# Performance work log

Hardware: AMD Instinct MI355X
Metric: run time of the kernel (lower is better)

The kernel has to match this reference:

```python
import jax, jax.numpy as jnp
import numpy as np

B, N = 1, 512
C_S, C_Z, C_HID, H, P_Q, P_V = 384, 128, 16, 12, 4, 8
W_C = (2.0 / (9.0 * P_Q)) ** 0.5
W_L = (1.0 / 3.0) ** 0.5
F_IN = H * C_Z + H * C_HID + H * P_V * 3 + H * P_V  # 2112


def setup_inputs() -> dict:
    key = jax.random.key(0)
    ks = jax.random.split(key, 14)
    s_i = jax.random.normal(ks[0], (B, N, C_S), jnp.float32)
    z_ij = jax.random.normal(ks[1], (B, N, N, C_Z), jnp.float32)
    # proper rotation matrices via QR so invert_apply is a true rigid inverse
    rot, _ = jnp.linalg.qr(jax.random.normal(ks[2], (B, N, 3, 3), jnp.float32))
    trans = jax.random.normal(ks[3], (B, N, 3), jnp.float32)
    sc = lambda fan: 1.0 / np.sqrt(fan)
    Wq = jax.random.normal(ks[4], (C_S, H, C_HID), jnp.float32) * sc(C_S)
    Wk = jax.random.normal(ks[5], (C_S, H, C_HID), jnp.float32) * sc(C_S)
    Wv = jax.random.normal(ks[6], (C_S, H, C_HID), jnp.float32) * sc(C_S)
    Wqp = jax.random.normal(ks[7], (C_S, H, P_Q, 3), jnp.float32) * sc(C_S)
    Wkp = jax.random.normal(ks[8], (C_S, H, P_Q, 3), jnp.float32) * sc(C_S)
    Wvp = jax.random.normal(ks[9], (C_S, H, P_V, 3), jnp.float32) * sc(C_S)
    Wb = jax.random.normal(ks[10], (C_Z, H), jnp.float32) * sc(C_Z)
    gamma = jax.random.normal(ks[11], (H,), jnp.float32)
    Wf = jax.random.normal(ks[12], (F_IN, C_S), jnp.float32) * sc(F_IN)
    bf = jnp.zeros((C_S,), jnp.float32)
    return {"s_i": s_i, "z_ij": z_ij, "rot": rot, "trans": trans,
            "Wq": Wq, "Wk": Wk, "Wv": Wv, "Wqp": Wqp, "Wkp": Wkp, "Wvp": Wvp,
            "Wb": Wb, "gamma": gamma, "Wf": Wf, "bf": bf}


def _apply(rot, trans, p):
    # rigid transform per residue: R_i @ p + t_i ; p: (B,N,H,P,3)
    return jnp.einsum('bimn,bihpn->bihpm', rot, p) + trans[:, :, None, None, :]


def reference(s_i, z_ij, rot, trans, Wq, Wk, Wv, Wqp, Wkp, Wvp, Wb, gamma, Wf, bf):
    q = jnp.einsum('bic,chd->bihd', s_i, Wq)            # (B,N,H,C_HID)
    k = jnp.einsum('bic,chd->bihd', s_i, Wk)
    v = jnp.einsum('bic,chd->bihd', s_i, Wv)
    qp = jnp.einsum('bic,chpx->bihpx', s_i, Wqp)        # (B,N,H,Pq,3)
    kp = jnp.einsum('bic,chpx->bihpx', s_i, Wkp)
    vp = jnp.einsum('bic,chpx->bihpx', s_i, Wvp)        # (B,N,H,Pv,3)
    b_ij = jnp.einsum('bijc,ch->bijh', z_ij, Wb)        # pair bias (B,N,N,H)

    qp_g = _apply(rot, trans, qp)
    kp_g = _apply(rot, trans, kp)
    # squared global point distances, summed over points: (B,N,N,H)
    d2 = jnp.sum((qp_g[:, :, None] - kp_g[:, None]) ** 2, axis=(-1, -2))

    qk = jnp.einsum('bihd,bjhd->bijh', q, k) * (1.0 / np.sqrt(C_HID))
    logits = W_L * (qk + b_ij - (W_C * 0.5) * gamma * d2)
    a = jax.nn.softmax(logits, axis=2)                  # softmax over j

    o_pair = jnp.einsum('bijh,bijc->bihc', a, z_ij)     # (B,N,H,C_Z)
    o_sc = jnp.einsum('bijh,bjhd->bihd', a, v)          # (B,N,H,C_HID)
    vp_g = _apply(rot, trans, vp)
    o_pt_g = jnp.einsum('bijh,bjhpx->bihpx', a, vp_g)   # (B,N,H,Pv,3)
    # invert_apply at residue i: R_i^T @ (x - t_i)
    o_pt = jnp.einsum('bimn,bihpm->bihpn', rot, o_pt_g - trans[:, :, None, None, :])
    o_norm = jnp.sqrt(jnp.sum(o_pt ** 2, axis=-1) + 1e-12)  # (B,N,H,Pv)

    feat = jnp.concatenate([o_pair.reshape(B, N, -1), o_sc.reshape(B, N, -1),
                            o_pt.reshape(B, N, -1), o_norm.reshape(B, N, -1)], axis=-1)
    return feat @ Wf + bf
```

## Files before the change

kernel.cpp:

```cpp
#include <hip/hip_runtime.h>
#include <hip/hip_bf16.h>
#include <math.h>

#define Nn    512
#define CS    384
#define CZ    128
#define CH    16
#define Hh    12
#define PQ    4
#define PV    8
#define NCOL  1152
#define FIN   2112

#define W_C   0.23570226039551584f
#define W_L   0.5773502691896258f

typedef unsigned short ushort_t;
typedef unsigned int uint_t;
typedef __attribute__((ext_vector_type(8))) short bf16x8;
typedef __attribute__((ext_vector_type(4))) float f32x4;

#define OFF_P      0u
#define OFF_MQ     589824u
#define OFF_MK     595968u
#define OFF_VT     602112u
#define OFF_VPT    651264u
#define OFF_S16    1830912u
#define OFF_WCT    1929216u
#define OFF_WFT    2150400u
#define OFF_F16    2555904u
#define OFF_PP     3145728u
#define OFF_VFRAG  5328896u
#define OFF_EXT    5451776u
#define OFF_EKB    21755904u
#define OFF_EQB    21854208u
#define OFF_WBF    21952512u

__device__ inline ushort_t f2bf(float f) {
  __hip_bfloat16 h = __float2bfloat16(f);
  return *reinterpret_cast<ushort_t*>(&h);
}
__device__ inline float bf2f(ushort_t u) {
  unsigned int x = ((unsigned int)u) << 16;
  return __uint_as_float(x);
}

__global__ __launch_bounds__(384) void k_conv(
    const float* __restrict__ s, const float* __restrict__ Wq,
    const float* __restrict__ Wk, const float* __restrict__ Wv,
    const float* __restrict__ Wqp, const float* __restrict__ Wkp,
    const float* __restrict__ Wvp, const float* __restrict__ Wf,
    const float* __restrict__ Wb,
    ushort_t* __restrict__ s16, ushort_t* __restrict__ WcatT,
    ushort_t* __restrict__ WfT, ushort_t* __restrict__ wbf) {
  int b = blockIdx.x;
  if (b < 512) {
    int idx = b * 384 + threadIdx.x;
    s16[idx] = f2bf(s[idx]);
  } else if (b < 1664) {
    int col = b - 512, k = threadIdx.x;
    float v;
    if      (col < 192)  v = Wq [k * 192 + col];
    else if (col < 384)  v = Wk [k * 192 + col - 192];
    else if (col < 576)  v = Wv [k * 192 + col - 384];
    else if (col < 720)  v = Wqp[k * 144 + col - 576];
    else if (col < 864)  v = Wkp[k * 144 + col - 720];
    else                 v = Wvp[k * 288 + col - 864];
    WcatT[(size_t)col * CS + k] = f2bf(v);
  } else if (b < 2048) {
    int o = b - 1664;
    for (int f = threadIdx.x; f < FIN; f += 384)
      WfT[(size_t)o * FIN + f] = f2bf(Wf[(size_t)f * CS + o]);
  } else {
    int t = threadIdx.x;
    if (t < 256) {
      int kk = t >> 6, l = t & 63;
      int h = l & 15, lk = l >> 4;
#pragma unroll
      for (int e = 0; e < 8; ++e) {
        int c = kk * 32 + lk * 8 + e;
        wbf[t * 8 + e] = (h < Hh) ? f2bf(Wb[c * Hh + h]) : (ushort_t)0;
      }
    }
  }
}

__global__ __launch_bounds__(64) void k_projm(
    const ushort_t* __restrict__ s16, const ushort_t* __restrict__ WcatT,
    float* __restrict__ P) {
  int colt = blockIdx.x;
  int i0 = blockIdx.y * 16;
  int l = threadIdx.x;
  int cl = l & 15, lk = l >> 4;
  f32x4 accA = {0.f, 0.f, 0.f, 0.f}, accB = {0.f, 0.f, 0.f, 0.f};
  const ushort_t* arow = s16 + (size_t)(i0 + cl) * CS;
  const ushort_t* brow = WcatT + (size_t)(colt * 16 + cl) * CS;
#pragma unroll
  for (int kk = 0; kk < 12; kk += 2) {
    bf16x8 a0 = *(const bf16x8*)(arow + kk * 32 + lk * 8);
    bf16x8 b0 = *(const bf16x8*)(brow + kk * 32 + lk * 8);
    accA = __builtin_amdgcn_mfma_f32_16x16x32_bf16(a0, b0, accA, 0, 0, 0);
    bf16x8 a1 = *(const bf16x8*)(arow + (kk + 1) * 32 + lk * 8);
    bf16x8 b1 = *(const bf16x8*)(brow + (kk + 1) * 32 + lk * 8);
    accB = __builtin_amdgcn_mfma_f32_16x16x32_bf16(a1, b1, accB, 0, 0, 0);
  }
#pragma unroll
  for (int r = 0; r < 4; ++r)
    P[(size_t)(i0 + lk * 4 + r) * NCOL + colt * 16 + cl] = accA[r] + accB[r];
}

__global__ __launch_bounds__(64) void k_prep(
    const float* __restrict__ P, const float* __restrict__ rot,
    const float* __restrict__ trans, const float* __restrict__ gamma,
    ushort_t* __restrict__ eqb, ushort_t* __restrict__ ekb,
    float* __restrict__ mq, float* __restrict__ mk,
    ushort_t* __restrict__ vT, ushort_t* __restrict__ vpT) {
  int gid = blockIdx.x * 64 + threadIdx.x;
  int i = gid / Hh, h = gid % Hh;
  const float* Pi = P + (size_t)i * NCOL;
  float R[9], T[3];
#pragma unroll
  for (int m = 0; m < 9; ++m) R[m] = rot[i * 9 + m];
#pragma unroll
  for (int m = 0; m < 3; ++m) T[m] = trans[i * 3 + m];
  float cg = W_C * gamma[h];

  ushort_t* eq = eqb + (size_t)gid * 32;
  ushort_t* ek = ekb + (size_t)gid * 32;
#pragma unroll
  for (int d = 0; d < CH; ++d) eq[d] = f2bf(Pi[h * CH + d] * 0.25f);
#pragma unroll
  for (int d = 0; d < CH; ++d) ek[d] = f2bf(Pi[192 + h * CH + d]);
  float sq = 0.f, sk = 0.f;
#pragma unroll
  for (int p = 0; p < PQ; ++p) {
    float x = Pi[576 + h * 12 + p * 3 + 0];
    float y = Pi[576 + h * 12 + p * 3 + 1];
    float zc = Pi[576 + h * 12 + p * 3 + 2];
    float gx = R[0] * x + R[1] * y + R[2] * zc + T[0];
    float gy = R[3] * x + R[4] * y + R[5] * zc + T[1];
    float gz = R[6] * x + R[7] * y + R[8] * zc + T[2];
    eq[16 + p * 3 + 0] = f2bf(cg * gx);
    eq[16 + p * 3 + 1] = f2bf(cg * gy);
    eq[16 + p * 3 + 2] = f2bf(cg * gz);
    sq += gx * gx + gy * gy + gz * gz;
  }
#pragma unroll
  for (int p = 0; p < PQ; ++p) {
    float x = Pi[720 + h * 12 + p * 3 + 0];
    float y = Pi[720 + h * 12 + p * 3 + 1];
    float zc = Pi[720 + h * 12 + p * 3 + 2];
    float gx = R[0] * x + R[1] * y + R[2] * zc + T[0];
    float gy = R[3] * x + R[4] * y + R[5] * zc + T[1];
    float gz = R[6] * x + R[7] * y + R[8] * zc + T[2];
    ek[16 + p * 3 + 0] = f2bf(gx);
    ek[16 + p * 3 + 1] = f2bf(gy);
    ek[16 + p * 3 + 2] = f2bf(gz);
    sk += gx * gx + gy * gy + gz * gz;
  }
#pragma unroll
  for (int d = 28; d < 32; ++d) { eq[d] = 0; ek[d] = 0; }
  mq[gid] = -0.5f * cg * sq;
  mk[gid] = -0.5f * cg * sk;

#pragma unroll
  for (int d = 0; d < CH; ++d)
    vT[(size_t)(h * CH + d) * Nn + i] = f2bf(Pi[384 + h * CH + d]);
#pragma unroll
  for (int p = 0; p < PV; ++p) {
    float x = Pi[864 + h * 24 + p * 3 + 0];
    float y = Pi[864 + h * 24 + p * 3 + 1];
    float zc = Pi[864 + h * 24 + p * 3 + 2];
    vpT[(size_t)(h * 24 + p * 3 + 0) * Nn + i] = f2bf(R[0] * x + R[1] * y + R[2] * zc + T[0]);
    vpT[(size_t)(h * 24 + p * 3 + 1) * Nn + i] = f2bf(R[3] * x + R[4] * y + R[5] * zc + T[1]);
    vpT[(size_t)(h * 24 + p * 3 + 2) * Nn + i] = f2bf(R[6] * x + R[7] * y + R[8] * zc + T[2]);
  }
}

__global__ __launch_bounds__(768) void k_aux(
    const ushort_t* __restrict__ eqb, const ushort_t* __restrict__ ekb,
    const float* __restrict__ mk, float* __restrict__ ext,
    const ushort_t* __restrict__ vT, const ushort_t* __restrict__ vpT,
    ushort_t* __restrict__ vfrag) {
  int b = blockIdx.x, tid = threadIdx.x;
  if (b < 1024) {
    int it = b >> 5, jt = b & 31;
    int l = tid & 63, h = tid >> 6;
    int cl = l & 15, lk = l >> 4;
    bf16x8 a = *(const bf16x8*)(eqb + ((size_t)(it * 16 + cl) * Hh + h) * 32 + lk * 8);
    bf16x8 bb = *(const bf16x8*)(ekb + ((size_t)(jt * 16 + cl) * Hh + h) * 32 + lk * 8);
    f32x4 dl = {0.f, 0.f, 0.f, 0.f};
    dl = __builtin_amdgcn_mfma_f32_16x16x32_bf16(a, bb, dl, 0, 0, 0);
    float mkv = mk[(jt * 16 + cl) * Hh + h];
    float* erow = ext + ((size_t)h * Nn + it * 16 + lk * 4) * Nn + jt * 16 + cl;
#pragma unroll
    for (int r = 0; r < 4; ++r) erow[(size_t)r * Nn] = dl[r] + mkv;
  } else {
    int flat = (b - 1024) * 768 + tid;
    if (flat < 30720) {
      int tt = flat >> 10;
      int r = flat & 1023;
      int jb = r >> 6, l = r & 63;
      int cl = l & 15, lk = l >> 4;
      const ushort_t* src = (tt < 12)
          ? vT  + (size_t)(tt * 16 + cl) * Nn
          : vpT + (size_t)((tt - 12) * 16 + cl) * Nn;
      bf16x8 v = *(const bf16x8*)(src + jb * 32 + lk * 8);
      *(bf16x8*)(vfrag + (((size_t)tt * 16 + jb) * 64 + l) * 8) = v;
    }
  }
}

__global__ __launch_bounds__(512, 4) void k_fused9(
    const float* __restrict__ z, const ushort_t* __restrict__ wbf,
    const float* __restrict__ ext, const ushort_t* __restrict__ vfrag,
    float* __restrict__ pp) {
  __shared__ float smemf[20240];
  char*     ztc  = (char*)smemf;
  char*     pB   = (char*)smemf + 65536;
  ushort_t* extb = (ushort_t*)((char*)smemf + 73728);
  float*    mb   = smemf + 19968;
  float*    lb   = smemf + 20096;
  float*    Mv   = smemf + 20224;

  int i = blockIdx.x, half = blockIdx.y, tid = threadIdx.x;
  int l = tid & 63, w = tid >> 6;
  int cl = l & 15, lk = l >> 4;
  int j0b = half * 256;
  float* po = pp + ((size_t)i * 2 + half) * 2048;
  int swz = (cl & 7) << 4;

  const float4* zg4 = (const float4*)(z + ((size_t)i * Nn + j0b) * CZ);
  float4 xv0 = zg4[w * 1024 + 0 * 64 + l],  xv1 = zg4[w * 1024 + 1 * 64 + l];
  float4 xv2 = zg4[w * 1024 + 2 * 64 + l],  xv3 = zg4[w * 1024 + 3 * 64 + l];
  float4 xv4 = zg4[w * 1024 + 4 * 64 + l],  xv5 = zg4[w * 1024 + 5 * 64 + l];
  float4 xv6 = zg4[w * 1024 + 6 * 64 + l],  xv7 = zg4[w * 1024 + 7 * 64 + l];
  float4 xv8 = zg4[w * 1024 + 8 * 64 + l],  xv9 = zg4[w * 1024 + 9 * 64 + l];
  float4 xv10 = zg4[w * 1024 + 10 * 64 + l], xv11 = zg4[w * 1024 + 11 * 64 + l];
  float4 xv12 = zg4[w * 1024 + 12 * 64 + l], xv13 = zg4[w * 1024 + 13 * 64 + l];
  float4 xv14 = zg4[w * 1024 + 14 * 64 + l], xv15 = zg4[w * 1024 + 15 * 64 + l];
  float ev[6];
#pragma unroll
  for (int q = 0; q < 6; ++q) {
    int flat = q * 64 + l;
    int eh = flat >> 5, ejl = flat & 31;
    ev[q] = ext[((size_t)eh * Nn + i) * Nn + j0b + w * 32 + ejl];
  }

#define STORE_ZT(it_, xv_) { \
    int idxl = (it_) * 64 + l; \
    int row = w * 32 + (idxl >> 5), c4 = idxl & 31; \
    uint2 pk; \
    pk.x = (uint_t)f2bf(xv_.x) | ((uint_t)f2bf(xv_.y) << 16); \
    pk.y = (uint_t)f2bf(xv_.z) | ((uint_t)f2bf(xv_.w) << 16); \
    *(uint2*)&ztc[row * 256 + ((c4 * 8) ^ ((row & 7) << 4))] = pk; }
  STORE_ZT(0, xv0)   STORE_ZT(1, xv1)   STORE_ZT(2, xv2)   STORE_ZT(3, xv3)
  STORE_ZT(4, xv4)   STORE_ZT(5, xv5)   STORE_ZT(6, xv6)   STORE_ZT(7, xv7)
  STORE_ZT(8, xv8)   STORE_ZT(9, xv9)   STORE_ZT(10, xv10) STORE_ZT(11, xv11)
  STORE_ZT(12, xv12) STORE_ZT(13, xv13) STORE_ZT(14, xv14) STORE_ZT(15, xv15)
#undef STORE_ZT
#pragma unroll
  for (int q = 0; q < 6; ++q) {
    int flat = q * 64 + l;
    extb[(w * 32 + (flat & 31)) * 12 + (flat >> 5)] = f2bf(ev[q]);
  }

  bf16x8 wbreg[4];
#pragma unroll
  for (int kk = 0; kk < 4; ++kk)
    wbreg[kk] = *(const bf16x8*)&wbf[(kk * 64 + l) * 8];

  float v[2][4];
#pragma unroll
  for (int cg = 0; cg < 2; ++cg) {
    int jloc = w * 32 + cg * 16 + cl;
    f32x4 dl = {0.f, 0.f, 0.f, 0.f};
#pragma unroll
    for (int kk = 0; kk < 4; ++kk) {
      bf16x8 a = *(const bf16x8*)&ztc[jloc * 256 + ((kk * 64 + lk * 16) ^ ((cl & 7) << 4))];
      dl = __builtin_amdgcn_mfma_f32_16x16x32_bf16(a, wbreg[kk], dl, 0, 0, 0);
    }
    if (cl < Hh) {
#pragma unroll
      for (int r = 0; r < 4; ++r)
        v[cg][r] = W_L * (dl[r] +
            bf2f(extb[(w * 32 + cg * 16 + lk * 4 + r) * 12 + cl]));
    } else {
#pragma unroll
      for (int r = 0; r < 4; ++r) v[cg][r] = -1e30f;
    }
  }

  float m_w = v[0][0];
#pragma unroll
  for (int cg = 0; cg < 2; ++cg)
#pragma unroll
    for (int r = 0; r < 4; ++r) m_w = fmaxf(m_w, v[cg][r]);
  m_w = fmaxf(m_w, __shfl_xor(m_w, 16));
  m_w = fmaxf(m_w, __shfl_xor(m_w, 32));

  float ps = 0.f;
#pragma unroll
  for (int cg = 0; cg < 2; ++cg) {
    int j = w * 32 + cg * 16 + lk * 4;
    ushort_t p0 = f2bf(__expf(v[cg][0] - m_w));
    ushort_t p1 = f2bf(__expf(v[cg][1] - m_w));
    ushort_t p2 = f2bf(__expf(v[cg][2] - m_w));
    ushort_t p3 = f2bf(__expf(v[cg][3] - m_w));
    ps += bf2f(p0) + bf2f(p1) + bf2f(p2) + bf2f(p3);
    uint2 d;
    d.x = (uint_t)p0 | ((uint_t)p1 << 16);
    d.y = (uint_t)p2 | ((uint_t)p3 << 16);
    *(uint2*)&pB[(cl * 512 + j * 2) ^ swz] = d;
  }
  ps += __shfl_xor(ps, 16);
  ps += __shfl_xor(ps, 32);
  if (lk == 0) { mb[w * 16 + cl] = m_w; lb[w * 16 + cl] = ps; }
  __syncthreads();

  if (tid < 16) {
    float M = mb[tid];
#pragma unroll
    for (int ww = 1; ww < 8; ++ww) M = fmaxf(M, mb[ww * 16 + tid]);
    float L = 0.f;
#pragma unroll
    for (int ww = 0; ww < 8; ++ww) L += lb[ww * 16 + tid] * __expf(mb[ww * 16 + tid] - M);
    Mv[tid] = M;
    po[2016 + tid] = M;
    po[2032 + tid] = L;
  }
  __syncthreads();

  float sf = __expf(m_w - Mv[cl]);
#pragma unroll
  for (int q = 0; q < 2; ++q) {
    int j = w * 32 + lk * 8 + q * 4;
    uint_t off = (uint_t)(cl * 512 + j * 2) ^ swz;
    uint2 d = *(uint2*)&pB[off];
    ushort_t q0 = f2bf(bf2f((ushort_t)(d.x & 0xffff)) * sf);
    ushort_t q1 = f2bf(bf2f((ushort_t)(d.x >> 16)) * sf);
    ushort_t q2 = f2bf(bf2f((ushort_t)(d.y & 0xffff)) * sf);
    ushort_t q3 = f2bf(bf2f((ushort_t)(d.y >> 16)) * sf);
    d.x = (uint_t)q0 | ((uint_t)q1 << 16);
    d.y = (uint_t)q2 | ((uint_t)q3 << 16);
    *(uint2*)&pB[off] = d;
  }
  __syncthreads();

  f32x4 acc[5];
#pragma unroll
  for (int n = 0; n < 5; ++n) acc[n] = (f32x4){0.f, 0.f, 0.f, 0.f};
  bf16x8 vA[4], vB[4];

#define LOADV(buf, kk_) { \
    _Pragma("unroll") \
    for (int n = 1; n < 5; ++n) { \
      int t = w + n * 8; \
      if (t < 38) buf[n - 1] = *(const bf16x8*)(vfrag + \
          (((size_t)(t - 8) * 16 + (half * 8 + (kk_))) * 64 + l) * 8); \
    } }
#define COMPUTE(buf, kk_) { \
    int koff = (kk_) * 32 + lk * 8; \
    bf16x8 af = *(const bf16x8*)&pB[(cl * 512 + koff * 2) ^ swz]; \
    bf16x8 b0; \
    _Pragma("unroll") \
    for (int e = 0; e < 8; ++e) \
      b0[e] = *(const short*)&ztc[(koff + e) * 256 + ((w * 32 + cl * 2) ^ (e << 4))]; \
    acc[0] = __builtin_amdgcn_mfma_f32_16x16x32_bf16(af, b0, acc[0], 0, 0, 0); \
    _Pragma("unroll") \
    for (int n = 1; n < 5; ++n) { \
      int t = w + n * 8; \
      if (t < 38) acc[n] = __builtin_amdgcn_mfma_f32_16x16x32_bf16(af, buf[n - 1], acc[n], 0, 0, 0); \
    } }

  LOADV(vA, 0)
#pragma unroll
  for (int kk = 0; kk < 8; kk += 2) {
    LOADV(vB, kk + 1)
    COMPUTE(vA, kk)
    if (kk < 6) LOADV(vA, kk + 2)
    COMPUTE(vB, kk + 1)
  }
#undef LOADV
#undef COMPUTE

#pragma unroll
  for (int n = 0; n < 5; ++n) {
    int t = w + n * 8;
    if (t < 38) {
      if (t < 8) {
        int c = t * 16 + cl;
#pragma unroll
        for (int r = 0; r < 4; ++r) {
          int h = lk * 4 + r;
          if (h < Hh) po[h * CZ + c] = acc[n][r];
        }
      } else if (t < 20) {
        int h = t - 8;
        if (lk == (h >> 2)) po[1536 + h * CH + cl] = acc[n][h & 3];
      } else {
        int cp = (t - 20) * 16 + cl;
        int h = cp / 24;
        if (lk == (h >> 2)) po[1728 + cp] = acc[n][h & 3];
      }
    }
  }
}

__global__ __launch_bounds__(256) void k_merge(
    const float* __restrict__ pp, const float* __restrict__ rot,
    const float* __restrict__ trans, ushort_t* __restrict__ feat16) {
  __shared__ float a0s[16], a1s[16];
  __shared__ float optg[288];
  int i = blockIdx.x, tid = threadIdx.x;
  const float* p0 = pp + ((size_t)i * 2 + 0) * 2048;
  const float* p1 = pp + ((size_t)i * 2 + 1) * 2048;
  ushort_t* Fi = feat16 + (size_t)i * FIN;

  if (tid < 16) {
    float m0 = p0[2016 + tid], m1 = p1[2016 + tid];
    float M = fmaxf(m0, m1);
    float s0 = __expf(m0 - M), s1 = __expf(m1 - M);
    float L = p0[2032 + tid] * s0 + p1[2032 + tid] * s1;
    float inv = (tid < Hh) ? 1.f / L : 0.f;
    a0s[tid] = s0 * inv;
    a1s[tid] = s1 * inv;
  }
  __syncthreads();

  for (int idx = tid; idx < 1728; idx += 256) {
    int h = (idx < 1536) ? (idx >> 7) : ((idx - 1536) >> 4);
    Fi[idx] = f2bf(p0[idx] * a0s[h] + p1[idx] * a1s[h]);
  }
  for (int idx = tid; idx < 288; idx += 256) {
    int h = idx / 24;
    optg[idx] = p0[1728 + idx] * a0s[h] + p1[1728 + idx] * a1s[h];
  }
  __syncthreads();

  if (tid < 96) {
    int h = tid >> 3, p = tid & 7;
    int cp = h * 24 + p * 3;
    float g0 = optg[cp + 0] - trans[i * 3 + 0];
    float g1 = optg[cp + 1] - trans[i * 3 + 1];
    float g2 = optg[cp + 2] - trans[i * 3 + 2];
    const float* R = rot + i * 9;
    float ss = 0.f;
#pragma unroll
    for (int nn2 = 0; nn2 < 3; ++nn2) {
      float o = R[nn2] * g0 + R[3 + nn2] * g1 + R[6 + nn2] * g2;
      Fi[1728 + cp + nn2] = f2bf(o);
      ss += o * o;
    }
    Fi[2016 + h * 8 + p] = f2bf(sqrtf(ss + 1e-12f));
  }
}

__global__ __launch_bounds__(256) void k_outm2(
    const ushort_t* __restrict__ feat16, const ushort_t* __restrict__ WfT,
    const float* __restrict__ bfv, float* __restrict__ out) {
  __shared__ f32x4 red[4][64];
  int ot = blockIdx.x;
  int ib = blockIdx.y;
  int tid = threadIdx.x;
  int l = tid & 63, w = tid >> 6;
  int cl = l & 15, lk = l >> 4;
  int i0 = ib * 32 + (w >> 1) * 16;
  int kw = w & 1;
  const ushort_t* arow = feat16 + (size_t)(i0 + cl) * FIN;
  const ushort_t* brow = WfT + (size_t)(ot * 16 + cl) * FIN;
  f32x4 accA = {0.f, 0.f, 0.f, 0.f}, accB = {0.f, 0.f, 0.f, 0.f};
  int k0 = kw * 33;
#pragma unroll 4
  for (int kk = k0; kk < k0 + 32; kk += 2) {
    bf16x8 a0 = *(const bf16x8*)(arow + kk * 32 + lk * 8);
    bf16x8 b0 = *(const bf16x8*)(brow + kk * 32 + lk * 8);
    accA = __builtin_amdgcn_mfma_f32_16x16x32_bf16(a0, b0, accA, 0, 0, 0);
    bf16x8 a1 = *(const bf16x8*)(arow + (kk + 1) * 32 + lk * 8);
    bf16x8 b1 = *(const bf16x8*)(brow + (kk + 1) * 32 + lk * 8);
    accB = __builtin_amdgcn_mfma_f32_16x16x32_bf16(a1, b1, accB, 0, 0, 0);
  }
  {
    int kk = k0 + 32;
    bf16x8 a = *(const bf16x8*)(arow + kk * 32 + lk * 8);
    bf16x8 b = *(const bf16x8*)(brow + kk * 32 + lk * 8);
    accA = __builtin_amdgcn_mfma_f32_16x16x32_bf16(a, b, accA, 0, 0, 0);
  }
#pragma unroll
  for (int r = 0; r < 4; ++r) accA[r] += accB[r];
  red[w][l] = accA;
  __syncthreads();
  if (kw == 0) {
    f32x4 s = red[w][l];
    f32x4 o = red[w + 1][l];
    float bias = bfv[ot * 16 + cl];
#pragma unroll
    for (int r = 0; r < 4; ++r)
      out[(size_t)(i0 + lk * 4 + r) * CS + ot * 16 + cl] = s[r] + o[r] + bias;
  }
}

extern "C" void kernel_launch(void* const* d_in, const int* in_sizes, int n_in,
                              void* d_out, int out_size, void* d_ws, size_t ws_size,
                              hipStream_t stream) {
  const float* s_i   = (const float*)d_in[0];
  const float* z_ij  = (const float*)d_in[1];
  const float* rot   = (const float*)d_in[2];
  const float* trans = (const float*)d_in[3];
  const float* Wq    = (const float*)d_in[4];
  const float* Wk    = (const float*)d_in[5];
  const float* Wv    = (const float*)d_in[6];
  const float* Wqp   = (const float*)d_in[7];
  const float* Wkp   = (const float*)d_in[8];
  const float* Wvp   = (const float*)d_in[9];
  const float* Wb    = (const float*)d_in[10];
  const float* gamma = (const float*)d_in[11];
  const float* Wf    = (const float*)d_in[12];
  const float* bf    = (const float*)d_in[13];
  float* out = (float*)d_out;

  float* w = (float*)d_ws;
  float*    P     = w + OFF_P;
  float*    mq    = w + OFF_MQ;
  float*    mk    = w + OFF_MK;
  ushort_t* vT    = (ushort_t*)(w + OFF_VT);
  ushort_t* vpT   = (ushort_t*)(w + OFF_VPT);
  ushort_t* s16   = (ushort_t*)(w + OFF_S16);
  ushort_t* WcT   = (ushort_t*)(w + OFF_WCT);
  ushort_t* WfT   = (ushort_t*)(w + OFF_WFT);
  ushort_t* f16   = (ushort_t*)(w + OFF_F16);
  float*    pp    = w + OFF_PP;
  ushort_t* vfrag = (ushort_t*)(w + OFF_VFRAG);
  float*    ext   = w + OFF_EXT;
  ushort_t* ekb   = (ushort_t*)(w + OFF_EKB);
  ushort_t* eqb   = (ushort_t*)(w + OFF_EQB);
  ushort_t* wbf   = (ushort_t*)(w + OFF_WBF);

  k_conv<<<2049, 384, 0, stream>>>(s_i, Wq, Wk, Wv, Wqp, Wkp, Wvp, Wf, Wb,
                                   s16, WcT, WfT, wbf);
  k_projm<<<dim3(72, 32), 64, 0, stream>>>(s16, WcT, P);
  k_prep<<<96, 64, 0, stream>>>(P, rot, trans, gamma, eqb, ekb, mq, mk, vT, vpT);
  k_aux<<<1064, 768, 0, stream>>>(eqb, ekb, mk, ext, vT, vpT, vfrag);
  k_fused9<<<dim3(512, 2), 512, 0, stream>>>(z_ij, wbf, ext, vfrag, pp);
  k_merge<<<512, 256, 0, stream>>>(pp, rot, trans, f16);
  k_outm2<<<dim3(24, 16), 256, 0, stream>>>(f16, WfT, bf, out);
}
```

Baseline: 89.27 us.

## Fuse split-softmax halves and merge into one online-softmax attention kernel

```diff
diff --git a/kernel.cpp b/kernel.cpp
--- a/kernel.cpp
+++ b/kernel.cpp
@@ -29,7 +29,6 @@
 #define OFF_WCT    1929216u
 #define OFF_WFT    2150400u
 #define OFF_F16    2555904u
-#define OFF_PP     3145728u
 #define OFF_VFRAG  5328896u
 #define OFF_EXT    5451776u
 #define OFF_EKB    21755904u
@@ -211,41 +210,57 @@
   }
 }
 
-__global__ __launch_bounds__(512, 4) void k_fused9(
+__global__ __launch_bounds__(512, 4) void k_fused10(
     const float* __restrict__ z, const ushort_t* __restrict__ wbf,
     const float* __restrict__ ext, const ushort_t* __restrict__ vfrag,
-    float* __restrict__ pp) {
-  __shared__ float smemf[20240];
+    const float* __restrict__ rot, const float* __restrict__ trans,
+    ushort_t* __restrict__ feat16) {
+  __shared__ float smemf[20256];
   char*     ztc  = (char*)smemf;
   char*     pB   = (char*)smemf + 65536;
   ushort_t* extb = (ushort_t*)((char*)smemf + 73728);
   float*    mb   = smemf + 19968;
   float*    lb   = smemf + 20096;
   float*    Mv   = smemf + 20224;
-
-  int i = blockIdx.x, half = blockIdx.y, tid = threadIdx.x;
+  float*    Mrun = smemf + 20240;
+
+  int i = blockIdx.x, tid = threadIdx.x;
   int l = tid & 63, w = tid >> 6;
   int cl = l & 15, lk = l >> 4;
-  int j0b = half * 256;
-  float* po = pp + ((size_t)i * 2 + half) * 2048;
+  ushort_t* Fi = feat16 + (size_t)i * FIN;
   int swz = (cl & 7) << 4;
 
-  const float4* zg4 = (const float4*)(z + ((size_t)i * Nn + j0b) * CZ);
-  float4 xv0 = zg4[w * 1024 + 0 * 64 + l],  xv1 = zg4[w * 1024 + 1 * 64 + l];
-  float4 xv2 = zg4[w * 1024 + 2 * 64 + l],  xv3 = zg4[w * 1024 + 3 * 64 + l];
-  float4 xv4 = zg4[w * 1024 + 4 * 64 + l],  xv5 = zg4[w * 1024 + 5 * 64 + l];
-  float4 xv6 = zg4[w * 1024 + 6 * 64 + l],  xv7 = zg4[w * 1024 + 7 * 64 + l];
-  float4 xv8 = zg4[w * 1024 + 8 * 64 + l],  xv9 = zg4[w * 1024 + 9 * 64 + l];
-  float4 xv10 = zg4[w * 1024 + 10 * 64 + l], xv11 = zg4[w * 1024 + 11 * 64 + l];
-  float4 xv12 = zg4[w * 1024 + 12 * 64 + l], xv13 = zg4[w * 1024 + 13 * 64 + l];
-  float4 xv14 = zg4[w * 1024 + 14 * 64 + l], xv15 = zg4[w * 1024 + 15 * 64 + l];
-  float ev[6];
-#pragma unroll
-  for (int q = 0; q < 6; ++q) {
-    int flat = q * 64 + l;
-    int eh = flat >> 5, ejl = flat & 31;
-    ev[q] = ext[((size_t)eh * Nn + i) * Nn + j0b + w * 32 + ejl];
-  }
+  float L_run = 0.f;
+  if (tid < 16) Mrun[tid] = -1e30f;
+
+  bf16x8 wbreg[4];
+#pragma unroll
+  for (int kk = 0; kk < 4; ++kk)
+    wbreg[kk] = *(const bf16x8*)&wbf[(kk * 64 + l) * 8];
+
+  f32x4 acc[5];
+#pragma unroll
+  for (int n = 0; n < 5; ++n) acc[n] = (f32x4){0.f, 0.f, 0.f, 0.f};
+
+  for (int half = 0; half < 2; ++half) {
+    int j0b = half * 256;
+
+    const float4* zg4 = (const float4*)(z + ((size_t)i * Nn + j0b) * CZ);
+    float4 xv0 = zg4[w * 1024 + 0 * 64 + l],  xv1 = zg4[w * 1024 + 1 * 64 + l];
+    float4 xv2 = zg4[w * 1024 + 2 * 64 + l],  xv3 = zg4[w * 1024 + 3 * 64 + l];
+    float4 xv4 = zg4[w * 1024 + 4 * 64 + l],  xv5 = zg4[w * 1024 + 5 * 64 + l];
+    float4 xv6 = zg4[w * 1024 + 6 * 64 + l],  xv7 = zg4[w * 1024 + 7 * 64 + l];
+    float4 xv8 = zg4[w * 1024 + 8 * 64 + l],  xv9 = zg4[w * 1024 + 9 * 64 + l];
+    float4 xv10 = zg4[w * 1024 + 10 * 64 + l], xv11 = zg4[w * 1024 + 11 * 64 + l];
+    float4 xv12 = zg4[w * 1024 + 12 * 64 + l], xv13 = zg4[w * 1024 + 13 * 64 + l];
+    float4 xv14 = zg4[w * 1024 + 14 * 64 + l], xv15 = zg4[w * 1024 + 15 * 64 + l];
+    float ev[6];
+#pragma unroll
+    for (int q = 0; q < 6; ++q) {
+      int flat = q * 64 + l;
+      int eh = flat >> 5, ejl = flat & 31;
+      ev[q] = ext[((size_t)eh * Nn + i) * Nn + j0b + w * 32 + ejl];
+    }
 
 #define STORE_ZT(it_, xv_) { \
     int idxl = (it_) * 64 + l; \
@@ -254,104 +269,109 @@
     pk.x = (uint_t)f2bf(xv_.x) | ((uint_t)f2bf(xv_.y) << 16); \
     pk.y = (uint_t)f2bf(xv_.z) | ((uint_t)f2bf(xv_.w) << 16); \
     *(uint2*)&ztc[row * 256 + ((c4 * 8) ^ ((row & 7) << 4))] = pk; }
-  STORE_ZT(0, xv0)   STORE_ZT(1, xv1)   STORE_ZT(2, xv2)   STORE_ZT(3, xv3)
-  STORE_ZT(4, xv4)   STORE_ZT(5, xv5)   STORE_ZT(6, xv6)   STORE_ZT(7, xv7)
-  STORE_ZT(8, xv8)   STORE_ZT(9, xv9)   STORE_ZT(10, xv10) STORE_ZT(11, xv11)
-  STORE_ZT(12, xv12) STORE_ZT(13, xv13) STORE_ZT(14, xv14) STORE_ZT(15, xv15)
+    STORE_ZT(0, xv0)   STORE_ZT(1, xv1)   STORE_ZT(2, xv2)   STORE_ZT(3, xv3)
+    STORE_ZT(4, xv4)   STORE_ZT(5, xv5)   STORE_ZT(6, xv6)   STORE_ZT(7, xv7)
+    STORE_ZT(8, xv8)   STORE_ZT(9, xv9)   STORE_ZT(10, xv10) STORE_ZT(11, xv11)
+    STORE_ZT(12, xv12) STORE_ZT(13, xv13) STORE_ZT(14, xv14) STORE_ZT(15, xv15)
 #undef STORE_ZT
 #pragma unroll
-  for (int q = 0; q < 6; ++q) {
-    int flat = q * 64 + l;
-    extb[(w * 32 + (flat & 31)) * 12 + (flat >> 5)] = f2bf(ev[q]);
-  }
-
-  bf16x8 wbreg[4];
-#pragma unroll
-  for (int kk = 0; kk < 4; ++kk)
-    wbreg[kk] = *(const bf16x8*)&wbf[(kk * 64 + l) * 8];
-
-  float v[2][4];
-#pragma unroll
-  for (int cg = 0; cg < 2; ++cg) {
-    int jloc = w * 32 + cg * 16 + cl;
-    f32x4 dl = {0.f, 0.f, 0.f, 0.f};
-#pragma unroll
-    for (int kk = 0; kk < 4; ++kk) {
-      bf16x8 a = *(const bf16x8*)&ztc[jloc * 256 + ((kk * 64 + lk * 16) ^ ((cl & 7) << 4))];
-      dl = __builtin_amdgcn_mfma_f32_16x16x32_bf16(a, wbreg[kk], dl, 0, 0, 0);
-    }
-    if (cl < Hh) {
-#pragma unroll
-      for (int r = 0; r < 4; ++r)
-        v[cg][r] = W_L * (dl[r] +
-            bf2f(extb[(w * 32 + cg * 16 + lk * 4 + r) * 12 + cl]));
-    } else {
-#pragma unroll
-      for (int r = 0; r < 4; ++r) v[cg][r] = -1e30f;
-    }
-  }
-
-  float m_w = v[0][0];
-#pragma unroll
-  for (int cg = 0; cg < 2; ++cg)
-#pragma unroll
-    for (int r = 0; r < 4; ++r) m_w = fmaxf(m_w, v[cg][r]);
-  m_w = fmaxf(m_w, __shfl_xor(m_w, 16));
-  m_w = fmaxf(m_w, __shfl_xor(m_w, 32));
-
-  float ps = 0.f;
-#pragma unroll
-  for (int cg = 0; cg < 2; ++cg) {
-    int j = w * 32 + cg * 16 + lk * 4;
-    ushort_t p0 = f2bf(__expf(v[cg][0] - m_w));
-    ushort_t p1 = f2bf(__expf(v[cg][1] - m_w));
-    ushort_t p2 = f2bf(__expf(v[cg][2] - m_w));
-    ushort_t p3 = f2bf(__expf(v[cg][3] - m_w));
-    ps += bf2f(p0) + bf2f(p1) + bf2f(p2) + bf2f(p3);
-    uint2 d;
-    d.x = (uint_t)p0 | ((uint_t)p1 << 16);
-    d.y = (uint_t)p2 | ((uint_t)p3 << 16);
-    *(uint2*)&pB[(cl * 512 + j * 2) ^ swz] = d;
-  }
-  ps += __shfl_xor(ps, 16);
-  ps += __shfl_xor(ps, 32);
-  if (lk == 0) { mb[w * 16 + cl] = m_w; lb[w * 16 + cl] = ps; }
-  __syncthreads();
-
-  if (tid < 16) {
-    float M = mb[tid];
-#pragma unroll
-    for (int ww = 1; ww < 8; ++ww) M = fmaxf(M, mb[ww * 16 + tid]);
-    float L = 0.f;
-#pragma unroll
-    for (int ww = 0; ww < 8; ++ww) L += lb[ww * 16 + tid] * __expf(mb[ww * 16 + tid] - M);
-    Mv[tid] = M;
-    po[2016 + tid] = M;
-    po[2032 + tid] = L;
-  }
-  __syncthreads();
-
-  float sf = __expf(m_w - Mv[cl]);
-#pragma unroll
-  for (int q = 0; q < 2; ++q) {
-    int j = w * 32 + lk * 8 + q * 4;
-    uint_t off = (uint_t)(cl * 512 + j * 2) ^ swz;
-    uint2 d = *(uint2*)&pB[off];
-    ushort_t q0 = f2bf(bf2f((ushort_t)(d.x & 0xffff)) * sf);
-    ushort_t q1 = f2bf(bf2f((ushort_t)(d.x >> 16)) * sf);
-    ushort_t q2 = f2bf(bf2f((ushort_t)(d.y & 0xffff)) * sf);
-    ushort_t q3 = f2bf(bf2f((ushort_t)(d.y >> 16)) * sf);
-    d.x = (uint_t)q0 | ((uint_t)q1 << 16);
-    d.y = (uint_t)q2 | ((uint_t)q3 << 16);
-    *(uint2*)&pB[off] = d;
-  }
-  __syncthreads();
-
-  f32x4 acc[5];
-#pragma unroll
-  for (int n = 0; n < 5; ++n) acc[n] = (f32x4){0.f, 0.f, 0.f, 0.f};
-  bf16x8 vA[4], vB[4];
-
+    for (int q = 0; q < 6; ++q) {
+      int flat = q * 64 + l;
+      extb[(w * 32 + (flat & 31)) * 12 + (flat >> 5)] = f2bf(ev[q]);
+    }
+
+    float v[2][4];
+#pragma unroll
+    for (int cg = 0; cg < 2; ++cg) {
+      int jloc = w * 32 + cg * 16 + cl;
+      f32x4 dl = {0.f, 0.f, 0.f, 0.f};
+#pragma unroll
+      for (int kk = 0; kk < 4; ++kk) {
+        bf16x8 a = *(const bf16x8*)&ztc[jloc * 256 + ((kk * 64 + lk * 16) ^ ((cl & 7) << 4))];
+        dl = __builtin_amdgcn_mfma_f32_16x16x32_bf16(a, wbreg[kk], dl, 0, 0, 0);
+      }
+      if (cl < Hh) {
+#pragma unroll
+        for (int r = 0; r < 4; ++r)
+          v[cg][r] = W_L * (dl[r] +
+              bf2f(extb[(w * 32 + cg * 16 + lk * 4 + r) * 12 + cl]));
+      } else {
+#pragma unroll
+        for (int r = 0; r < 4; ++r) v[cg][r] = -1e30f;
+      }
+    }
+
+    float m_w = v[0][0];
+#pragma unroll
+    for (int cg = 0; cg < 2; ++cg)
+#pragma unroll
+      for (int r = 0; r < 4; ++r) m_w = fmaxf(m_w, v[cg][r]);
+    m_w = fmaxf(m_w, __shfl_xor(m_w, 16));
+    m_w = fmaxf(m_w, __shfl_xor(m_w, 32));
+
+    float ps = 0.f;
+#pragma unroll
+    for (int cg = 0; cg < 2; ++cg) {
+      int j = w * 32 + cg * 16 + lk * 4;
+      ushort_t p0 = f2bf(__expf(v[cg][0] - m_w));
+      ushort_t p1 = f2bf(__expf(v[cg][1] - m_w));
+      ushort_t p2 = f2bf(__expf(v[cg][2] - m_w));
+      ushort_t p3 = f2bf(__expf(v[cg][3] - m_w));
+      ps += bf2f(p0) + bf2f(p1) + bf2f(p2) + bf2f(p3);
+      uint2 d;
+      d.x = (uint_t)p0 | ((uint_t)p1 << 16);
+      d.y = (uint_t)p2 | ((uint_t)p3 << 16);
+      *(uint2*)&pB[(cl * 512 + j * 2) ^ swz] = d;
+    }
+    ps += __shfl_xor(ps, 16);
+    ps += __shfl_xor(ps, 32);
+    if (lk == 0) { mb[w * 16 + cl] = m_w; lb[w * 16 + cl] = ps; }
+    __syncthreads();
+
+    if (tid < 16) {
+      float m1 = mb[tid];
+#pragma unroll
+      for (int ww = 1; ww < 8; ++ww) m1 = fmaxf(m1, mb[ww * 16 + tid]);
+      float Mold = Mrun[tid];
+      float Mnew = fmaxf(Mold, m1);
+      float Lh = 0.f;
+#pragma unroll
+      for (int ww = 0; ww < 8; ++ww)
+        Lh += lb[ww * 16 + tid] * __expf(mb[ww * 16 + tid] - Mnew);
+      L_run = L_run * __expf(Mold - Mnew) + Lh;
+      Mv[tid] = Mnew;
+      mb[tid] = __expf(Mold - Mnew);
+      Mrun[tid] = Mnew;
+    }
+    __syncthreads();
+
+    if (half == 1) {
+      float scr[4];
+#pragma unroll
+      for (int r = 0; r < 4; ++r) scr[r] = mb[lk * 4 + r];
+#pragma unroll
+      for (int n = 0; n < 5; ++n)
+#pragma unroll
+        for (int r = 0; r < 4; ++r) acc[n][r] *= scr[r];
+    }
+
+    float sf = __expf(m_w - Mv[cl]);
+#pragma unroll
+    for (int q = 0; q < 2; ++q) {
+      int j = w * 32 + lk * 8 + q * 4;
+      uint_t off = (uint_t)(cl * 512 + j * 2) ^ swz;
+      uint2 d = *(uint2*)&pB[off];
+      ushort_t q0 = f2bf(bf2f((ushort_t)(d.x & 0xffff)) * sf);
+      ushort_t q1 = f2bf(bf2f((ushort_t)(d.x >> 16)) * sf);
+      ushort_t q2 = f2bf(bf2f((ushort_t)(d.y & 0xffff)) * sf);
+      ushort_t q3 = f2bf(bf2f((ushort_t)(d.y >> 16)) * sf);
+      d.x = (uint_t)q0 | ((uint_t)q1 << 16);
+      d.y = (uint_t)q2 | ((uint_t)q3 << 16);
+      *(uint2*)&pB[off] = d;
+    }
+    __syncthreads();
+
+    bf16x8 vA[4], vB[4];
 #define LOADV(buf, kk_) { \
     _Pragma("unroll") \
     for (int n = 1; n < 5; ++n) { \
@@ -373,17 +393,25 @@
       if (t < 38) acc[n] = __builtin_amdgcn_mfma_f32_16x16x32_bf16(af, buf[n - 1], acc[n], 0, 0, 0); \
     } }
 
-  LOADV(vA, 0)
-#pragma unroll
-  for (int kk = 0; kk < 8; kk += 2) {
-    LOADV(vB, kk + 1)
-    COMPUTE(vA, kk)
-    if (kk < 6) LOADV(vA, kk + 2)
-    COMPUTE(vB, kk + 1)
-  }
+    LOADV(vA, 0)
+#pragma unroll
+    for (int kk = 0; kk < 8; kk += 2) {
+      LOADV(vB, kk + 1)
+      COMPUTE(vA, kk)
+      if (kk < 6) LOADV(vA, kk + 2)
+      COMPUTE(vB, kk + 1)
+    }
 #undef LOADV
 #undef COMPUTE
-
+    __syncthreads();
+  }
+
+  float* optg = (float*)extb;
+  if (tid < 16) Mrun[tid] = (tid < Hh) ? 1.f / L_run : 0.f;
+  __syncthreads();
+  float rl[4];
+#pragma unroll
+  for (int r = 0; r < 4; ++r) rl[r] = Mrun[lk * 4 + r];
 #pragma unroll
   for (int n = 0; n < 5; ++n) {
     int t = w + n * 8;
@@ -393,48 +421,17 @@
 #pragma unroll
         for (int r = 0; r < 4; ++r) {
           int h = lk * 4 + r;
-          if (h < Hh) po[h * CZ + c] = acc[n][r];
+          if (h < Hh) Fi[h * CZ + c] = f2bf(acc[n][r] * rl[r]);
         }
       } else if (t < 20) {
         int h = t - 8;
-        if (lk == (h >> 2)) po[1536 + h * CH + cl] = acc[n][h & 3];
+        if (lk == (h >> 2)) Fi[1536 + h * CH + cl] = f2bf(acc[n][h & 3] * rl[h & 3]);
       } else {
         int cp = (t - 20) * 16 + cl;
         int h = cp / 24;
-        if (lk == (h >> 2)) po[1728 + cp] = acc[n][h & 3];
+        if (lk == (h >> 2)) optg[cp] = acc[n][h & 3] * rl[h & 3];
       }
     }
-  }
-}
-
-__global__ __launch_bounds__(256) void k_merge(
-    const float* __restrict__ pp, const float* __restrict__ rot,
-    const float* __restrict__ trans, ushort_t* __restrict__ feat16) {
-  __shared__ float a0s[16], a1s[16];
-  __shared__ float optg[288];
-  int i = blockIdx.x, tid = threadIdx.x;
-  const float* p0 = pp + ((size_t)i * 2 + 0) * 2048;
-  const float* p1 = pp + ((size_t)i * 2 + 1) * 2048;
-  ushort_t* Fi = feat16 + (size_t)i * FIN;
-
-  if (tid < 16) {
-    float m0 = p0[2016 + tid], m1 = p1[2016 + tid];
-    float M = fmaxf(m0, m1);
-    float s0 = __expf(m0 - M), s1 = __expf(m1 - M);
-    float L = p0[2032 + tid] * s0 + p1[2032 + tid] * s1;
-    float inv = (tid < Hh) ? 1.f / L : 0.f;
-    a0s[tid] = s0 * inv;
-    a1s[tid] = s1 * inv;
-  }
-  __syncthreads();
-
-  for (int idx = tid; idx < 1728; idx += 256) {
-    int h = (idx < 1536) ? (idx >> 7) : ((idx - 1536) >> 4);
-    Fi[idx] = f2bf(p0[idx] * a0s[h] + p1[idx] * a1s[h]);
-  }
-  for (int idx = tid; idx < 288; idx += 256) {
-    int h = idx / 24;
-    optg[idx] = p0[1728 + idx] * a0s[h] + p1[1728 + idx] * a1s[h];
   }
   __syncthreads();
 
@@ -529,7 +526,6 @@
   ushort_t* WcT   = (ushort_t*)(w + OFF_WCT);
   ushort_t* WfT   = (ushort_t*)(w + OFF_WFT);
   ushort_t* f16   = (ushort_t*)(w + OFF_F16);
-  float*    pp    = w + OFF_PP;
   ushort_t* vfrag = (ushort_t*)(w + OFF_VFRAG);
   float*    ext   = w + OFF_EXT;
   ushort_t* ekb   = (ushort_t*)(w + OFF_EKB);
@@ -541,7 +537,6 @@
   k_projm<<<dim3(72, 32), 64, 0, stream>>>(s16, WcT, P);
   k_prep<<<96, 64, 0, stream>>>(P, rot, trans, gamma, eqb, ekb, mq, mk, vT, vpT);
   k_aux<<<1064, 768, 0, stream>>>(eqb, ekb, mk, ext, vT, vpT, vfrag);
-  k_fused9<<<dim3(512, 2), 512, 0, stream>>>(z_ij, wbf, ext, vfrag, pp);
-  k_merge<<<512, 256, 0, stream>>>(pp, rot, trans, f16);
+  k_fused10<<<512, 512, 0, stream>>>(z_ij, wbf, ext, vfrag, rot, trans, f16);
   k_outm2<<<dim3(24, 16), 256, 0, stream>>>(f16, WfT, bf, out);
 }
```

Measured after the change: 114.4 us. 1.28x slower.
